# Kernel optimization log

Hardware: AMD Instinct MI355X
Metric: run time of the kernel (lower is better)

Reference implementation:

```python
import jax, jax.numpy as jnp
import numpy as np

D_MODEL = 512
EXPAND = 2
D_INNER = EXPAND * D_MODEL      # 1024
D_STATE = 16
D_CONV = 4
DT_RANK = (D_MODEL + 15) // 16  # 32
B, L = 2, 2048


def _mamba(x, in_w, conv_w, conv_b, xproj_w, dt_w, dt_b, A_log, D_skip, out_w):
    """Single-direction Mamba mixer. x: (B,L,d_model)."""
    xz = x @ in_w                              # (B,L,2*Di)
    xi, z = jnp.split(xz, 2, axis=-1)          # (B,L,Di) each
    # causal depthwise conv1d, kernel size D_CONV
    xp = jnp.pad(xi, ((0, 0), (D_CONV - 1, 0), (0, 0)))
    Ls = xi.shape[1]
    conv = sum(conv_w[:, k] * xp[:, k:k + Ls, :] for k in range(D_CONV))
    xc = jax.nn.silu(conv + conv_b)            # (B,L,Di)
    dbc = xc @ xproj_w                         # (B,L,dt_rank+2*N)
    dt = dbc[..., :DT_RANK]
    Bc = dbc[..., DT_RANK:DT_RANK + D_STATE]   # (B,L,N)
    Cc = dbc[..., DT_RANK + D_STATE:]          # (B,L,N)
    dt = jax.nn.softplus(dt @ dt_w + dt_b)     # (B,L,Di)
    A = -jnp.exp(A_log)                        # (Di,N)
    dA = jnp.exp(dt[..., None] * A)            # (B,L,Di,N)
    dBx = (dt * xc)[..., None] * Bc[:, :, None, :]  # (B,L,Di,N)

    def comb(e1, e2):
        a1, b1 = e1
        a2, b2 = e2
        return a2 * a1, a2 * b1 + b2

    _, h = jax.lax.associative_scan(comb, (dA, dBx), axis=1)  # (B,L,Di,N)
    y = jnp.einsum('bldn,bln->bld', h, Cc) + xc * D_skip
    y = y * jax.nn.silu(z)
    return y @ out_w                           # (B,L,d_model)


def setup_inputs() -> dict:
    key = jax.random.key(0)
    ks = jax.random.split(key, 20)
    f32 = jnp.float32
    s = 0.02

    def mixer(kk):
        k = jax.random.split(kk, 8)
        return dict(
            in_w=jax.random.normal(k[0], (D_MODEL, 2 * D_INNER), f32) * s,
            conv_w=jax.random.normal(k[1], (D_INNER, D_CONV), f32) * 0.2,
            conv_b=jnp.zeros((D_INNER,), f32),
            xproj_w=jax.random.normal(k[2], (D_INNER, DT_RANK + 2 * D_STATE), f32) * s,
            dt_w=jax.random.normal(k[3], (DT_RANK, D_INNER), f32) * s,
            dt_b=jnp.full((D_INNER,), np.log(np.expm1(0.01)), f32),
            A_log=jnp.log(jnp.broadcast_to(jnp.arange(1, D_STATE + 1, dtype=f32), (D_INNER, D_STATE))),
            D_skip=jnp.ones((D_INNER,), f32),
            out_w=jax.random.normal(k[4], (D_INNER, D_MODEL), f32) * s,
        )

    fwd = mixer(ks[1])
    bwd = mixer(ks[2])
    inp = {'hidden_states': jax.random.normal(ks[0], (B, L, D_MODEL), f32)}
    for name, p in [('fwd', fwd), ('bwd', bwd)]:
        for k2, v in p.items():
            inp[f'{name}_{k2}'] = v
    inp['fuse_w'] = jax.random.normal(ks[3], (2 * D_MODEL, D_MODEL), f32) * s
    inp['fuse_b'] = jnp.zeros((D_MODEL,), f32)
    return inp


def reference(hidden_states,
              fwd_in_w, fwd_conv_w, fwd_conv_b, fwd_xproj_w, fwd_dt_w, fwd_dt_b,
              fwd_A_log, fwd_D_skip, fwd_out_w,
              bwd_in_w, bwd_conv_w, bwd_conv_b, bwd_xproj_w, bwd_dt_w, bwd_dt_b,
              bwd_A_log, bwd_D_skip, bwd_out_w,
              fuse_w, fuse_b):
    out_fwd = _mamba(hidden_states, fwd_in_w, fwd_conv_w, fwd_conv_b, fwd_xproj_w,
                     fwd_dt_w, fwd_dt_b, fwd_A_log, fwd_D_skip, fwd_out_w)
    xr = jnp.flip(hidden_states, axis=1)
    out_rev = _mamba(xr, bwd_in_w, bwd_conv_w, bwd_conv_b, bwd_xproj_w,
                     bwd_dt_w, bwd_dt_b, bwd_A_log, bwd_D_skip, bwd_out_w)
    out_rev = jnp.flip(out_rev, axis=1)
    combined = jnp.concatenate([out_fwd, out_rev], axis=-1)
    # dropout is identity in eval mode
    return combined @ fuse_w + fuse_b
```

## Files before the change

kernel.cpp:

```cpp
#include <hip/hip_runtime.h>
#include <hip/hip_bf16.h>


#define DM 512
#define DI 1024
#define DS 16
#define DCV 4
#define DTR 32
#define BB 2
#define LL 2048
#define NTOK (BB * LL)

#define T_CHUNK 16
#define NCHUNK (LL / T_CHUNK)

#define XC_D ((size_t)NTOK * DI)
#define DBC_D ((size_t)NTOK * 64)
#define ST_D ((size_t)BB * NCHUNK * DI * DS)
#define SDT_D ((size_t)BB * NCHUNK * DI)
#define Y_D ((size_t)NTOK * DI)
#define OP_D ((size_t)NTOK * DM)

#define CONV_TT 8

typedef unsigned short ushortT;
typedef unsigned int u32;
typedef __attribute__((ext_vector_type(8))) short short8;
typedef __attribute__((ext_vector_type(4))) float floatx4;
typedef __attribute__((ext_vector_type(4))) unsigned short ushort4T;

#define LOG2E 1.4426950408889634f

__device__ __forceinline__ float silu_f(float v) {
    return v / (1.f + __expf(-v));
}

__device__ __forceinline__ ushortT f2bf(float f) {
    union { float f; u32 u; } v; v.f = f;
    u32 u = v.u;
    u32 r = (u + 0x7fffu + ((u >> 16) & 1u)) >> 16;
    return (ushortT)r;
}
__device__ __forceinline__ float bf2f(ushortT h) {
    union { float f; u32 u; } v; v.u = ((u32)h) << 16; return v.f;
}

__device__ __forceinline__ void load_lds16(const ushortT* g, ushortT* l) {
    __builtin_amdgcn_global_load_lds((const __attribute__((address_space(1))) u32*)g,
                                     (__attribute__((address_space(3))) u32*)l, 16, 0, 0);
}

__device__ __forceinline__ void do_split4(const float* __restrict__ src,
                                          ushortT* __restrict__ H, ushortT* __restrict__ L,
                                          size_t i) {
    float4 v = *(const float4*)&src[i];
    ushortT h0 = f2bf(v.x), h1 = f2bf(v.y), h2 = f2bf(v.z), h3 = f2bf(v.w);
    H[i + 0] = h0; H[i + 1] = h1; H[i + 2] = h2; H[i + 3] = h3;
    L[i + 0] = f2bf(v.x - bf2f(h0));
    L[i + 1] = f2bf(v.y - bf2f(h1));
    L[i + 2] = f2bf(v.z - bf2f(h2));
    L[i + 3] = f2bf(v.w - bf2f(h3));
}

__device__ __forceinline__ void do_transpose(const float* __restrict__ W,
                                             ushortT* __restrict__ Wh, ushortT* __restrict__ Wl,
                                             int K, int N, int kb, int nb, int tid,
                                             float (*t)[33]) {
    int r = tid / 8, c = (tid % 8) * 4;
    float4 v = *(const float4*)&W[(size_t)(kb + r) * N + nb + c];
    t[r][c + 0] = v.x; t[r][c + 1] = v.y; t[r][c + 2] = v.z; t[r][c + 3] = v.w;
    __syncthreads();
#pragma unroll
    for (int i = 0; i < 4; ++i) {
        float x = t[c + i][r];
        ushortT h = f2bf(x);
        size_t o = (size_t)(nb + r) * K + kb + c + i;
        Wh[o] = h;
        Wl[o] = f2bf(x - bf2f(h));
    }
}

__launch_bounds__(256)
__global__ void prep(const float* __restrict__ x, const float* __restrict__ fuse_w,
                     const float* __restrict__ iw0, const float* __restrict__ iw1,
                     const float* __restrict__ ow0, const float* __restrict__ ow1,
                     const float* __restrict__ dw0, const float* __restrict__ dw1,
                     const float* __restrict__ xw0, const float* __restrict__ xw1,
                     ushortT* __restrict__ xh, ushortT* __restrict__ xl,
                     ushortT* __restrict__ fth, ushortT* __restrict__ ftl,
                     ushortT* __restrict__ wtih, ushortT* __restrict__ wtil,
                     ushortT* __restrict__ opwh, ushortT* __restrict__ opwl,
                     ushortT* __restrict__ wdth, ushortT* __restrict__ wdtl,
                     ushortT* __restrict__ wxh, ushortT* __restrict__ wxl) {
    __shared__ float t[32][33];
    const int bid = blockIdx.x;
    const int tid = threadIdx.x;

    if (bid < 2048) {
        do_split4(x, xh, xl, (size_t)bid * 1024 + tid * 4);
    } else if (bid < 2560) {
        int r = bid - 2048;
        do_transpose(fuse_w, fth, ftl, 2 * DM, DM, (r / 16) * 32, (r % 16) * 32, tid, t);
    } else if (bid < 4608) {
        int r = bid - 2560;
        int dir = r >> 10; r &= 1023;
        const float* w = dir ? iw1 : iw0;
        size_t off = (size_t)dir * DM * 2 * DI;
        do_transpose(w, wtih + off, wtil + off, DM, 2 * DI, (r / 64) * 32, (r % 64) * 32, tid, t);
    } else if (bid < 5632) {
        int r = bid - 4608;
        int dir = r >> 9; r &= 511;
        const float* w = dir ? ow1 : ow0;
        size_t off = (size_t)dir * DI * DM;
        do_split4(w, opwh + off, opwl + off, (size_t)r * 1024 + tid * 4);
    } else if (bid < 5696) {
        int r = bid - 5632;
        int dir = r >> 5; r &= 31;
        const float* w = dir ? dw1 : dw0;
        size_t off = (size_t)dir * DI * DTR;
        do_transpose(w, wdth + off, wdtl + off, DTR, DI, 0, r * 32, tid, t);
    } else {
        int r = bid - 5696;
        int dir = r >> 6; r &= 63;
        const float* w = dir ? xw1 : xw0;
        size_t off = (size_t)dir * 64 * DI;
        do_transpose(w, wxh + off, wxl + off, DI, 64, (r / 2) * 32, (r % 2) * 32, tid, t);
    }
}

template <int BM, int BN, int WM, int WN, int OUTMODE, int SPLITK = 1, int CATREV = 0,
          int ZONLY = 0, int SWAPXY = 0>
__launch_bounds__(256)
__global__ void gemm_bf16s(const ushortT* __restrict__ Ahi, const ushortT* __restrict__ Alo, size_t Aoff,
                           const ushortT* __restrict__ Bhi, const ushortT* __restrict__ Blo, size_t Boff,
                           float* __restrict__ C, size_t Coff,
                           const float* __restrict__ bias0, const float* __restrict__ bias1,
                           ushortT* __restrict__ Chi, ushortT* __restrict__ Clo, size_t CoOff,
                           int M, int N, int K, int lda, int ldc, int revA, int revC) {
    constexpr int BK = 32;
    constexpr int MI = WM / 16, NI = WN / 16;
    __shared__ ushortT sAh[BM * BK], sBh[BN * BK];
    __shared__ ushortT sAl[ZONLY ? 1 : BM * BK], sBl[ZONLY ? 1 : BN * BK];

    const int dir = blockIdx.z / SPLITK;
    if (!CATREV) { Ahi += dir * Aoff; Alo += dir * Aoff; }
    Bhi += dir * Boff; Blo += dir * Boff;
    const float* bias = dir ? bias1 : bias0;
    if (OUTMODE == 4) {
        C += (size_t)blockIdx.z * Coff;
    } else if (OUTMODE == 2) {
        Chi += dir * CoOff; Clo += dir * CoOff;
    } else if (OUTMODE == 5) {
        Chi += dir * CoOff;
    } else {
        C += dir * Coff;
    }
    const int kz = blockIdx.z % SPLITK;
    const int rA = revA & dir, rC = revC & dir;

    const int tid = threadIdx.x;
    const int wave = tid >> 6, lane = tid & 63;
    const int wm = wave >> 1, wn = wave & 1;
    const int m0 = (SWAPXY ? blockIdx.x : blockIdx.y) * BM;
    const int n0 = (SWAPXY ? blockIdx.y : blockIdx.x) * BN;
    const int quad = lane >> 4, l16 = lane & 15;
    const int srow = lane >> 2;
    const int scolg = (((lane & 3) ^ (srow & 3)) * 8);

    floatx4 acc[MI][NI] = {};

    const int klen = K / SPLITK;
    for (int k0 = kz * klen; k0 < (kz + 1) * klen; k0 += BK) {
        __syncthreads();
#pragma unroll
        for (int s = wave; s < BM / 16; s += 4) {
            int gm = m0 + s * 16 + srow;
            int grow = gm;
            size_t base = 0;
            if (CATREV) {
                if (k0 >= (K >> 1)) {
                    int b = gm >> 11; int t = gm & 2047; grow = (b << 11) + (2047 - t);
                    base = Aoff - (size_t)(K >> 1);
                }
            } else if (rA) {
                int b = gm >> 11; int t = gm & 2047; grow = (b << 11) + (2047 - t);
            }
            size_t goff = base + (size_t)grow * lda + k0 + scolg;
            load_lds16(Ahi + goff, sAh + s * 16 * BK);
            if (!ZONLY) load_lds16(Alo + goff, sAl + s * 16 * BK);
        }
#pragma unroll
        for (int s = wave; s < BN / 16; s += 4) {
            int gn = n0 + s * 16 + srow;
            size_t goff = (size_t)gn * K + k0 + scolg;
            load_lds16(Bhi + goff, sBh + s * 16 * BK);
            if (!ZONLY) load_lds16(Blo + goff, sBl + s * 16 * BK);
        }
        __syncthreads();

        short8 ah[MI], al[MI], bh[NI], bl[NI];
#pragma unroll
        for (int i = 0; i < MI; ++i) {
            int r = wm * WM + i * 16 + l16;
            int co = (quad ^ (r & 3)) * 8;
            ah[i] = *(const short8*)(sAh + r * BK + co);
            if (!ZONLY) al[i] = *(const short8*)(sAl + r * BK + co);
        }
#pragma unroll
        for (int j = 0; j < NI; ++j) {
            int r = wn * WN + j * 16 + l16;
            int co = (quad ^ (r & 3)) * 8;
            bh[j] = *(const short8*)(sBh + r * BK + co);
            if (!ZONLY) bl[j] = *(const short8*)(sBl + r * BK + co);
        }
#pragma unroll
        for (int i = 0; i < MI; ++i)
#pragma unroll
            for (int j = 0; j < NI; ++j) {
                acc[i][j] = __builtin_amdgcn_mfma_f32_16x16x32_bf16(ah[i], bh[j], acc[i][j], 0, 0, 0);
                if (!ZONLY) {
                    acc[i][j] = __builtin_amdgcn_mfma_f32_16x16x32_bf16(al[i], bh[j], acc[i][j], 0, 0, 0);
                    acc[i][j] = __builtin_amdgcn_mfma_f32_16x16x32_bf16(ah[i], bl[j], acc[i][j], 0, 0, 0);
                }
            }
    }

#pragma unroll
    for (int i = 0; i < MI; ++i) {
#pragma unroll
        for (int r = 0; r < 4; ++r) {
            int gm = m0 + wm * WM + i * 16 + quad * 4 + r;
            int grow = gm;
            if (rC) { int b = gm >> 11; int t = gm & 2047; grow = (b << 11) + (2047 - t); }
#pragma unroll
            for (int j = 0; j < NI; ++j) {
                int gn = n0 + wn * WN + j * 16 + l16;
                float v = acc[i][j][r];
                if (OUTMODE == 1 || OUTMODE == 3) v += bias[gn];
                if (OUTMODE == 3) v = (v > 20.f) ? v : log1pf(__expf(v));
                if (OUTMODE == 2) {
                    ushortT h = f2bf(v);
                    size_t o = (size_t)grow * ldc + gn;
                    Chi[o] = h;
                    Clo[o] = f2bf(v - bf2f(h));
                } else if (OUTMODE == 5) {
                    Chi[(size_t)grow * ldc + gn] = f2bf(v);
                } else {
                    C[(size_t)grow * ldc + gn] = v;
                }
            }
        }
    }
}

__launch_bounds__(256)
__global__ void reduce_dbc(const float* __restrict__ xpp, float* __restrict__ dbc,
                           ushortT* __restrict__ dtAh, ushortT* __restrict__ dtAl) {
    const int dir = blockIdx.y;
    int idx = blockIdx.x * 256 + threadIdx.x;
    int row = idx >> 4;
    int c4 = (idx & 15) * 4;
    float4 s = {0.f, 0.f, 0.f, 0.f};
#pragma unroll
    for (int kz = 0; kz < 4; ++kz) {
        float4 v = *(const float4*)&xpp[(size_t)(dir * 4 + kz) * NTOK * 64 + (size_t)row * 64 + c4];
        s.x += v.x; s.y += v.y; s.z += v.z; s.w += v.w;
    }
    *(float4*)&dbc[dir * DBC_D + (size_t)row * 64 + c4] = s;
    if (c4 < DTR) {
        size_t o = (size_t)dir * NTOK * DTR + (size_t)row * DTR + c4;
        ushortT h0 = f2bf(s.x), h1 = f2bf(s.y), h2 = f2bf(s.z), h3 = f2bf(s.w);
        dtAh[o + 0] = h0; dtAh[o + 1] = h1; dtAh[o + 2] = h2; dtAh[o + 3] = h3;
        dtAl[o + 0] = f2bf(s.x - bf2f(h0));
        dtAl[o + 1] = f2bf(s.y - bf2f(h1));
        dtAl[o + 2] = f2bf(s.z - bf2f(h2));
        dtAl[o + 3] = f2bf(s.w - bf2f(h3));
    }
}

__launch_bounds__(256)
__global__ void reduce_out(const float* __restrict__ op, const float* __restrict__ bias,
                           float* __restrict__ out) {
    size_t i = ((size_t)blockIdx.x * 256 + threadIdx.x) * 4;
    float4 a = *(const float4*)&op[i];
    float4 b = *(const float4*)&op[OP_D + i];
    float4 bb = *(const float4*)&bias[(int)(i % DM)];
    float4 r = {a.x + b.x + bb.x, a.y + b.y + bb.y, a.z + b.z + bb.z, a.w + b.w + bb.w};
    *(float4*)&out[i] = r;
}

__launch_bounds__(256)
__global__ void conv_silu(const float* __restrict__ xz,
                          const float* __restrict__ cw0, const float* __restrict__ cw1,
                          const float* __restrict__ cb0, const float* __restrict__ cb1,
                          ushortT* __restrict__ xch, ushortT* __restrict__ xcl) {
    const int dir = blockIdx.y;
    const float* conv_w = dir ? cw1 : cw0;
    const float* conv_b = dir ? cb1 : cb0;
    xz += (size_t)dir * XC_D;
    xch += (size_t)dir * XC_D;
    xcl += (size_t)dir * XC_D;

    const int tid = threadIdx.x;
    const int c4 = tid * 4;
    const int chunk = blockIdx.x % (LL / CONV_TT);
    const int b = blockIdx.x / (LL / CONV_TT);
    const int t0 = chunk * CONV_TT;

    float4 w0 = *(const float4*)&conv_w[(c4 + 0) * DCV];
    float4 w1 = *(const float4*)&conv_w[(c4 + 1) * DCV];
    float4 w2 = *(const float4*)&conv_w[(c4 + 2) * DCV];
    float4 w3 = *(const float4*)&conv_w[(c4 + 3) * DCV];
    const float4 bias = *(const float4*)&conv_b[c4];

    const float* rowp = &xz[((size_t)b * LL + t0) * DI + c4];
    const float4 zero = {0.f, 0.f, 0.f, 0.f};
    float4 xm3 = (t0 >= 3) ? *(const float4*)(rowp - 3 * DI) : zero;
    float4 xm2 = (t0 >= 2) ? *(const float4*)(rowp - 2 * DI) : zero;
    float4 xm1 = (t0 >= 1) ? *(const float4*)(rowp - 1 * DI) : zero;

    ushortT* hp = &xch[((size_t)b * LL + t0) * DI + c4];
    ushortT* lp = &xcl[((size_t)b * LL + t0) * DI + c4];

#pragma unroll
    for (int t = 0; t < CONV_TT; ++t) {
        float4 cur = *(const float4*)(rowp + (size_t)t * DI);
        float y0 = bias.x + w0.x * xm3.x + w0.y * xm2.x + w0.z * xm1.x + w0.w * cur.x;
        float y1 = bias.y + w1.x * xm3.y + w1.y * xm2.y + w1.z * xm1.y + w1.w * cur.y;
        float y2 = bias.z + w2.x * xm3.z + w2.y * xm2.z + w2.z * xm1.z + w2.w * cur.z;
        float y3 = bias.w + w3.x * xm3.w + w3.y * xm2.w + w3.z * xm1.w + w3.w * cur.w;

        float v0 = silu_f(y0), v1 = silu_f(y1), v2 = silu_f(y2), v3 = silu_f(y3);
        ushortT h0 = f2bf(v0), h1 = f2bf(v1), h2 = f2bf(v2), h3 = f2bf(v3);
        ushort4T hv = {h0, h1, h2, h3};
        ushort4T lv = {f2bf(v0 - bf2f(h0)), f2bf(v1 - bf2f(h1)),
                       f2bf(v2 - bf2f(h2)), f2bf(v3 - bf2f(h3))};
        *(ushort4T*)(hp + (size_t)t * DI) = hv;
        *(ushort4T*)(lp + (size_t)t * DI) = lv;

        xm3 = xm2; xm2 = xm1; xm1 = cur;
    }
}

__launch_bounds__(256, 8)
__global__ void scan_phaseA(const float* __restrict__ dtv,
                            const ushortT* __restrict__ xch, const ushortT* __restrict__ xcl,
                            const float* __restrict__ dbc,
                            const float* __restrict__ Al0, const float* __restrict__ Al1,
                            float* __restrict__ sdtb,
                            float* __restrict__ hend) {
    const int dir = blockIdx.y;
    const float* A_log = dir ? Al1 : Al0;
    dtv += dir * XC_D;
    xch += dir * XC_D;
    xcl += dir * XC_D;
    dbc += dir * DBC_D;
    sdtb += dir * SDT_D;
    hend += dir * ST_D;

    const int cg = blockIdx.x % (DI / 256);
    const int j = (blockIdx.x / (DI / 256)) % NCHUNK;
    const int b = blockIdx.x / ((DI / 256) * NCHUNK);
    const int c = cg * 256 + threadIdx.x;

    const float A2b = -__expf(A_log[c * DS]) * LOG2E;

    float h[DS] = {};
    float sdt = 0.f;

    const int tokbase = b * LL + j * T_CHUNK;
#pragma unroll 2
    for (int t = 0; t < T_CHUNK; ++t) {
        size_t tok = tokbase + t;
        size_t o = tok * DI + c;
        float dt = dtv[o];
        float x  = bf2f(xch[o]) + bf2f(xcl[o]);
        float4 B0 = *(const float4*)&dbc[tok * 64 + DTR + 0];
        float4 B1 = *(const float4*)&dbc[tok * 64 + DTR + 4];
        float4 B2 = *(const float4*)&dbc[tok * 64 + DTR + 8];
        float4 B3 = *(const float4*)&dbc[tok * 64 + DTR + 12];
        float Bf[DS] = {B0.x, B0.y, B0.z, B0.w, B1.x, B1.y, B1.z, B1.w,
                        B2.x, B2.y, B2.z, B2.w, B3.x, B3.y, B3.z, B3.w};
        float u = dt * x;
        sdt += dt;
        float r = exp2f(dt * A2b);
        float dAacc = r;
#pragma unroll
        for (int n = 0; n < DS; ++n) {
            h[n] = dAacc * h[n] + u * Bf[n];
            dAacc *= r;
        }
    }

    size_t base = ((size_t)(b * NCHUNK + j) * DI + c) * DS;
#pragma unroll
    for (int q = 0; q < 4; ++q) {
        float4 hv = {h[q * 4], h[q * 4 + 1], h[q * 4 + 2], h[q * 4 + 3]};
        *(float4*)&hend[base + q * 4] = hv;
    }
    sdtb[(size_t)(b * NCHUNK + j) * DI + c] = sdt;
}

__launch_bounds__(256)
__global__ void scan_phaseB(const float* __restrict__ sdtb,
                            float* __restrict__ hend,
                            const float* __restrict__ Al0, const float* __restrict__ Al1) {
    const int dir = blockIdx.y;
    const float* A_log = dir ? Al1 : Al0;
    sdtb += dir * SDT_D;
    hend += dir * ST_D;
    int idx = blockIdx.x * 256 + threadIdx.x;
    int b = idx / (DI * DS);
    int p = idx % (DI * DS);
    int c = p >> 4;
    int n = p & 15;
    const float A2 = -__expf(A_log[c * DS]) * LOG2E * (float)(n + 1);
    float h = 0.f;
#pragma unroll 4
    for (int j = 0; j < NCHUNK; ++j) {
        float s = sdtb[(size_t)(b * NCHUNK + j) * DI + c];
        size_t o = ((size_t)(b * NCHUNK + j) * DI) * DS + p;
        float a = exp2f(s * A2);
        float e = hend[o];
        hend[o] = h;
        h = a * h + e;
    }
}

__launch_bounds__(256, 8)
__global__ void scan_phaseC(const float* __restrict__ dtv,
                            const ushortT* __restrict__ xch, const ushortT* __restrict__ xcl,
                            const float* __restrict__ dbc,
                            const ushortT* __restrict__ zh,
                            const float* __restrict__ Al0, const float* __restrict__ Al1,
                            const float* __restrict__ Dk0, const float* __restrict__ Dk1,
                            const float* __restrict__ hin,
                            ushortT* __restrict__ yh,
                            ushortT* __restrict__ yl) {
    const int dir = blockIdx.y;
    const float* A_log = dir ? Al1 : Al0;
    const float* Dskip = dir ? Dk1 : Dk0;
    dtv += dir * XC_D;
    xch += dir * XC_D;
    xcl += dir * XC_D;
    dbc += dir * DBC_D;
    zh += dir * XC_D;
    hin += dir * ST_D;
    yh += dir * Y_D;
    yl += dir * Y_D;

    const int cg = blockIdx.x % (DI / 256);
    const int j = (blockIdx.x / (DI / 256)) % NCHUNK;
    const int b = blockIdx.x / ((DI / 256) * NCHUNK);
    const int c = cg * 256 + threadIdx.x;
    const float Dsk = Dskip[c];
    const float A2b = -__expf(A_log[c * DS]) * LOG2E;

    float h[DS];
    size_t hbase = ((size_t)(b * NCHUNK + j) * DI + c) * DS;
#pragma unroll
    for (int q = 0; q < 4; ++q) {
        float4 hv = *(const float4*)&hin[hbase + q * 4];
        h[q * 4 + 0] = hv.x; h[q * 4 + 1] = hv.y;
        h[q * 4 + 2] = hv.z; h[q * 4 + 3] = hv.w;
    }

    const int tokbase = b * LL + j * T_CHUNK;
#pragma unroll 2
    for (int t = 0; t < T_CHUNK; ++t) {
        size_t tok = tokbase + t;
        size_t o = tok * DI + c;
        float dt = dtv[o];
        float x  = bf2f(xch[o]) + bf2f(xcl[o]);
        float4 B0 = *(const float4*)&dbc[tok * 64 + DTR + 0];
        float4 B1 = *(const float4*)&dbc[tok * 64 + DTR + 4];
        float4 B2 = *(const float4*)&dbc[tok * 64 + DTR + 8];
        float4 B3 = *(const float4*)&dbc[tok * 64 + DTR + 12];
        float4 C0 = *(const float4*)&dbc[tok * 64 + DTR + DS + 0];
        float4 C1 = *(const float4*)&dbc[tok * 64 + DTR + DS + 4];
        float4 C2 = *(const float4*)&dbc[tok * 64 + DTR + DS + 8];
        float4 C3 = *(const float4*)&dbc[tok * 64 + DTR + DS + 12];
        float Bf[DS] = {B0.x, B0.y, B0.z, B0.w, B1.x, B1.y, B1.z, B1.w,
                        B2.x, B2.y, B2.z, B2.w, B3.x, B3.y, B3.z, B3.w};
        float Cf[DS] = {C0.x, C0.y, C0.z, C0.w, C1.x, C1.y, C1.z, C1.w,
                        C2.x, C2.y, C2.z, C2.w, C3.x, C3.y, C3.z, C3.w};
        float u = dt * x;
        float r = exp2f(dt * A2b);
        float dAacc = r;
        float ysum = 0.f;
#pragma unroll
        for (int n = 0; n < DS; ++n) {
            h[n] = dAacc * h[n] + u * Bf[n];
            ysum += h[n] * Cf[n];
            dAacc *= r;
        }
        float zv = bf2f(zh[o]);
        float y = (ysum + x * Dsk) * silu_f(zv);
        ushortT hh = f2bf(y);
        yh[o] = hh;
        yl[o] = f2bf(y - bf2f(hh));
    }
}

extern "C" void kernel_launch(void* const* d_in, const int* in_sizes, int n_in,
                              void* d_out, int out_size, void* d_ws, size_t ws_size,
                              hipStream_t stream) {
    const float* x = (const float*)d_in[0];
    const float* fuse_w = (const float*)d_in[19];
    const float* fuse_b = (const float*)d_in[20];
    float* out = (float*)d_out;

    const float* in_w[2], *conv_w[2], *conv_b[2], *xproj_w[2], *dt_w[2], *dt_b[2],
               *A_log[2], *D_skip[2], *out_w[2];
    for (int dir = 0; dir < 2; ++dir) {
        in_w[dir]    = (const float*)d_in[1 + dir * 9 + 0];
        conv_w[dir]  = (const float*)d_in[1 + dir * 9 + 1];
        conv_b[dir]  = (const float*)d_in[1 + dir * 9 + 2];
        xproj_w[dir] = (const float*)d_in[1 + dir * 9 + 3];
        dt_w[dir]    = (const float*)d_in[1 + dir * 9 + 4];
        dt_b[dir]    = (const float*)d_in[1 + dir * 9 + 5];
        A_log[dir]   = (const float*)d_in[1 + dir * 9 + 6];
        D_skip[dir]  = (const float*)d_in[1 + dir * 9 + 7];
        out_w[dir]   = (const float*)d_in[1 + dir * 9 + 8];
    }

    char* p = (char*)d_ws;
    auto alloc = [&](size_t bytes) { char* r = p; p += (bytes + 255) & ~(size_t)255; return r; };

    float* xz    = (float*)alloc(2 * XC_D * 4);
    float* dtv   = (float*)alloc(2 * XC_D * 4);
    float* xpp   = dtv;
    float* opart = dtv;
    float* dbc   = (float*)alloc(2 * DBC_D * 4);
    float* hend  = (float*)alloc(2 * ST_D * 4);
    float* sdtb  = (float*)alloc(2 * SDT_D * 4);
    ushortT* zh   = (ushortT*)alloc(2 * XC_D * 2);
    ushortT* xh   = (ushortT*)alloc((size_t)NTOK * DM * 2);
    ushortT* xl   = (ushortT*)alloc((size_t)NTOK * DM * 2);
    ushortT* wtih = (ushortT*)alloc(2 * (size_t)DM * 2 * DI * 2);
    ushortT* wtil = (ushortT*)alloc(2 * (size_t)DM * 2 * DI * 2);
    ushortT* opwh = (ushortT*)alloc(2 * (size_t)DI * DM * 2);
    ushortT* opwl = (ushortT*)alloc(2 * (size_t)DI * DM * 2);
    ushortT* w1th = (ushortT*)alloc(2 * (size_t)DM * DI * 2);
    ushortT* w1tl = (ushortT*)alloc(2 * (size_t)DM * DI * 2);
    ushortT* fth  = (ushortT*)alloc((size_t)DM * 2 * DM * 2);
    ushortT* ftl  = (ushortT*)alloc((size_t)DM * 2 * DM * 2);
    ushortT* wdth = (ushortT*)alloc(2 * (size_t)DI * DTR * 2);
    ushortT* wdtl = (ushortT*)alloc(2 * (size_t)DI * DTR * 2);
    ushortT* wxh  = (ushortT*)alloc(2 * (size_t)64 * DI * 2);
    ushortT* wxl  = (ushortT*)alloc(2 * (size_t)64 * DI * 2);
    ushortT* dtAh = (ushortT*)alloc(2 * (size_t)NTOK * DTR * 2);
    ushortT* dtAl = (ushortT*)alloc(2 * (size_t)NTOK * DTR * 2);
    ushortT* yh   = (ushortT*)alloc(2 * Y_D * 2);
    ushortT* yl   = (ushortT*)alloc(2 * Y_D * 2);
    ushortT* xch  = yh;
    ushortT* xcl  = yl;

    prep<<<5824, 256, 0, stream>>>(x, fuse_w, in_w[0], in_w[1], out_w[0], out_w[1],
                                   dt_w[0], dt_w[1], xproj_w[0], xproj_w[1],
                                   xh, xl, fth, ftl, wtih, wtil, opwh, opwl,
                                   wdth, wdtl, wxh, wxl);

    gemm_bf16s<64, 64, 32, 32, 2><<<dim3(DI / 64, DM / 64, 2), 256, 0, stream>>>(
        fth, ftl, (size_t)DM, opwh, opwl, (size_t)DI * DM,
        nullptr, 0, nullptr, nullptr, w1th, w1tl, (size_t)DM * DI,
        DM, DI, DM, 2 * DM, DI, 0, 0);

    gemm_bf16s<128, 128, 64, 64, 0><<<dim3(DI / 128, NTOK / 128, 2), 256, 0, stream>>>(
        xh, xl, 0, wtih, wtil, (size_t)DM * 2 * DI, xz, XC_D, nullptr, nullptr,
        nullptr, nullptr, 0, NTOK, DI, DM, DM, DI, 1, 0);

    gemm_bf16s<128, 128, 64, 64, 5, 1, 0, 1><<<dim3(DI / 128, NTOK / 128, 2), 256, 0, stream>>>(
        xh, xl, 0, wtih + (size_t)DI * DM, wtil, (size_t)DM * 2 * DI, nullptr, 0,
        nullptr, nullptr, zh, nullptr, XC_D, NTOK, DI, DM, DM, DI, 1, 0);

    conv_silu<<<dim3(BB * (LL / CONV_TT), 2), 256, 0, stream>>>(
        xz, conv_w[0], conv_w[1], conv_b[0], conv_b[1], xch, xcl);

    gemm_bf16s<64, 64, 32, 32, 4, 4><<<dim3(1, NTOK / 64, 8), 256, 0, stream>>>(
        xch, xcl, XC_D, wxh, wxl, (size_t)64 * DI, xpp, (size_t)NTOK * 64,
        nullptr, nullptr, nullptr, nullptr, 0, NTOK, 64, DI, DI, 64, 0, 0);
    reduce_dbc<<<dim3(NTOK * 16 / 256, 2), 256, 0, stream>>>(xpp, dbc, dtAh, dtAl);

    gemm_bf16s<64, 64, 32, 32, 3><<<dim3(DI / 64, NTOK / 64, 2), 256, 0, stream>>>(
        dtAh, dtAl, (size_t)NTOK * DTR, wdth, wdtl, (size_t)DI * DTR,
        dtv, XC_D, dt_b[0], dt_b[1],
        nullptr, nullptr, 0, NTOK, DI, DTR, DTR, DI, 0, 0);

    scan_phaseA<<<dim3(BB * NCHUNK * (DI / 256), 2), 256, 0, stream>>>(
        dtv, xch, xcl, dbc, A_log[0], A_log[1], sdtb, hend);
    scan_phaseB<<<dim3(BB * DI * DS / 256, 2), 256, 0, stream>>>(
        sdtb, hend, A_log[0], A_log[1]);
    scan_phaseC<<<dim3(BB * NCHUNK * (DI / 256), 2), 256, 0, stream>>>(
        dtv, xch, xcl, dbc, zh, A_log[0], A_log[1], D_skip[0], D_skip[1], hend, yh, yl);

    gemm_bf16s<128, 64, 64, 32, 4, 1, 0, 0, 1><<<dim3(NTOK / 128, DM / 64, 2), 256, 0, stream>>>(
        yh, yl, Y_D, w1th, w1tl, (size_t)DM * DI, opart, OP_D,
        nullptr, nullptr, nullptr, nullptr, 0, NTOK, DM, DI, DI, DM, 1, 0);

    reduce_out<<<NTOK * DM / 1024, 256, 0, stream>>>(opart, fuse_b, out);
}
```

Measured before the change: 337.4 us.

## Fuse in_proj x/z GEMMs, extend LDS swizzle, split-K out projection

Merges the two in_proj GEMM launches (x part in split-bf16 fp32 output, z part in hi-only bf16) into one launch with a new output mode. Per block it picks whether to run the lo-precision MFMAs, based on whether the column tile lies in the x half. The LDS XOR swizzle now also mixes in row bits 2-3, aiming to cut bank conflicts on the short8 reads. The final out-projection GEMM uses split-K 2 with four z-slices, and reduce_out sums four partial buffers, which raises occupancy at the cost of extra partial-buffer traffic.

```diff
diff --git a/kernel.cpp b/kernel.cpp
--- a/kernel.cpp
+++ b/kernel.cpp
@@ -152,6 +152,8 @@
         Chi += dir * CoOff; Clo += dir * CoOff;
     } else if (OUTMODE == 5) {
         Chi += dir * CoOff;
+    } else if (OUTMODE == 6) {
+        C += dir * Coff; Chi += dir * CoOff;
     } else {
         C += dir * Coff;
     }
@@ -165,7 +167,9 @@
     const int n0 = (SWAPXY ? blockIdx.y : blockIdx.x) * BN;
     const int quad = lane >> 4, l16 = lane & 15;
     const int srow = lane >> 2;
-    const int scolg = (((lane & 3) ^ (srow & 3)) * 8);
+    const int scolg = (((lane & 3) ^ (srow & 3) ^ ((srow >> 2) & 3)) * 8);
+
+    const bool lo_on = (OUTMODE == 6) ? (n0 < DI) : (ZONLY == 0);
 
     floatx4 acc[MI][NI] = {};
 
@@ -187,14 +191,14 @@
             }
             size_t goff = base + (size_t)grow * lda + k0 + scolg;
             load_lds16(Ahi + goff, sAh + s * 16 * BK);
-            if (!ZONLY) load_lds16(Alo + goff, sAl + s * 16 * BK);
+            if (lo_on) load_lds16(Alo + goff, sAl + s * 16 * BK);
         }
 #pragma unroll
         for (int s = wave; s < BN / 16; s += 4) {
             int gn = n0 + s * 16 + srow;
             size_t goff = (size_t)gn * K + k0 + scolg;
             load_lds16(Bhi + goff, sBh + s * 16 * BK);
-            if (!ZONLY) load_lds16(Blo + goff, sBl + s * 16 * BK);
+            if (lo_on) load_lds16(Blo + goff, sBl + s * 16 * BK);
         }
         __syncthreads();
 
@@ -202,23 +206,23 @@
 #pragma unroll
         for (int i = 0; i < MI; ++i) {
             int r = wm * WM + i * 16 + l16;
-            int co = (quad ^ (r & 3)) * 8;
+            int co = ((quad ^ (r & 3) ^ ((r >> 2) & 3)) & 3) * 8;
             ah[i] = *(const short8*)(sAh + r * BK + co);
-            if (!ZONLY) al[i] = *(const short8*)(sAl + r * BK + co);
+            if (lo_on) al[i] = *(const short8*)(sAl + r * BK + co);
         }
 #pragma unroll
         for (int j = 0; j < NI; ++j) {
             int r = wn * WN + j * 16 + l16;
-            int co = (quad ^ (r & 3)) * 8;
+            int co = ((quad ^ (r & 3) ^ ((r >> 2) & 3)) & 3) * 8;
             bh[j] = *(const short8*)(sBh + r * BK + co);
-            if (!ZONLY) bl[j] = *(const short8*)(sBl + r * BK + co);
+            if (lo_on) bl[j] = *(const short8*)(sBl + r * BK + co);
         }
 #pragma unroll
         for (int i = 0; i < MI; ++i)
 #pragma unroll
             for (int j = 0; j < NI; ++j) {
                 acc[i][j] = __builtin_amdgcn_mfma_f32_16x16x32_bf16(ah[i], bh[j], acc[i][j], 0, 0, 0);
-                if (!ZONLY) {
+                if (lo_on) {
                     acc[i][j] = __builtin_amdgcn_mfma_f32_16x16x32_bf16(al[i], bh[j], acc[i][j], 0, 0, 0);
                     acc[i][j] = __builtin_amdgcn_mfma_f32_16x16x32_bf16(ah[i], bl[j], acc[i][j], 0, 0, 0);
                 }
@@ -245,6 +249,9 @@
                     Clo[o] = f2bf(v - bf2f(h));
                 } else if (OUTMODE == 5) {
                     Chi[(size_t)grow * ldc + gn] = f2bf(v);
+                } else if (OUTMODE == 6) {
+                    if (gn < DI) C[(size_t)grow * ldc + gn] = v;
+                    else Chi[(size_t)grow * ldc + (gn - DI)] = f2bf(v);
                 } else {
                     C[(size_t)grow * ldc + gn] = v;
                 }
@@ -284,8 +291,11 @@
     size_t i = ((size_t)blockIdx.x * 256 + threadIdx.x) * 4;
     float4 a = *(const float4*)&op[i];
     float4 b = *(const float4*)&op[OP_D + i];
+    float4 c = *(const float4*)&op[2 * OP_D + i];
+    float4 d = *(const float4*)&op[3 * OP_D + i];
     float4 bb = *(const float4*)&bias[(int)(i % DM)];
-    float4 r = {a.x + b.x + bb.x, a.y + b.y + bb.y, a.z + b.z + bb.z, a.w + b.w + bb.w};
+    float4 r = {a.x + b.x + c.x + d.x + bb.x, a.y + b.y + c.y + d.y + bb.y,
+                a.z + b.z + c.z + d.z + bb.z, a.w + b.w + c.w + d.w + bb.w};
     *(float4*)&out[i] = r;
 }
 
@@ -566,13 +576,9 @@
         nullptr, 0, nullptr, nullptr, w1th, w1tl, (size_t)DM * DI,
         DM, DI, DM, 2 * DM, DI, 0, 0);
 
-    gemm_bf16s<128, 128, 64, 64, 0><<<dim3(DI / 128, NTOK / 128, 2), 256, 0, stream>>>(
+    gemm_bf16s<128, 128, 64, 64, 6><<<dim3(2 * DI / 128, NTOK / 128, 2), 256, 0, stream>>>(
         xh, xl, 0, wtih, wtil, (size_t)DM * 2 * DI, xz, XC_D, nullptr, nullptr,
-        nullptr, nullptr, 0, NTOK, DI, DM, DM, DI, 1, 0);
-
-    gemm_bf16s<128, 128, 64, 64, 5, 1, 0, 1><<<dim3(DI / 128, NTOK / 128, 2), 256, 0, stream>>>(
-        xh, xl, 0, wtih + (size_t)DI * DM, wtil, (size_t)DM * 2 * DI, nullptr, 0,
-        nullptr, nullptr, zh, nullptr, XC_D, NTOK, DI, DM, DM, DI, 1, 0);
+        zh, nullptr, XC_D, NTOK, 2 * DI, DM, DM, DI, 1, 0);
 
     conv_silu<<<dim3(BB * (LL / CONV_TT), 2), 256, 0, stream>>>(
         xz, conv_w[0], conv_w[1], conv_b[0], conv_b[1], xch, xcl);
@@ -594,7 +600,7 @@
     scan_phaseC<<<dim3(BB * NCHUNK * (DI / 256), 2), 256, 0, stream>>>(
         dtv, xch, xcl, dbc, zh, A_log[0], A_log[1], D_skip[0], D_skip[1], hend, yh, yl);
 
-    gemm_bf16s<128, 64, 64, 32, 4, 1, 0, 0, 1><<<dim3(NTOK / 128, DM / 64, 2), 256, 0, stream>>>(
+    gemm_bf16s<128, 64, 64, 32, 4, 2, 0, 0, 1><<<dim3(NTOK / 128, DM / 64, 4), 256, 0, stream>>>(
         yh, yl, Y_D, w1th, w1tl, (size_t)DM * DI, opart, OP_D,
         nullptr, nullptr, nullptr, nullptr, 0, NTOK, DM, DI, DI, DM, 1, 0);
 
```

New measurement: 356.8 us. 5.8% more time.
